# Kernel tuning notes

Measured on AMD Instinct MI355X. Metric: run time of the kernel, lower is better.

## Reference

```python
import jax, jax.numpy as jnp
import numpy as np

B, D_IN, D_OUT, M = 4096, 1024, 1024, 16
GAMMA = 2.0


def setup_inputs() -> dict:
    key = jax.random.key(0)
    ks = jax.random.split(key, 5)
    scale_in = 1.0 / np.sqrt(D_IN)
    return {
        "x": jax.random.normal(ks[0], (B, D_IN), dtype=jnp.float32),
        "W": jax.random.normal(ks[1], (M, D_IN, D_OUT), dtype=jnp.float32) * scale_in,
        "b": jax.random.normal(ks[2], (M, D_OUT), dtype=jnp.float32) * 0.01,
        "Wg": jax.random.normal(ks[3], (D_IN, M), dtype=jnp.float32) * scale_in,
        "bg": jax.random.normal(ks[4], (M,), dtype=jnp.float32) * 0.01,
    }


def reference(x, W, b, Wg, bg):
    # Gate: linear -> pow(gamma) -> normalize by row sum -> relu
    gu = x @ Wg + bg                                   # [B, M]
    gp = jnp.power(gu, GAMMA)                          # gamma = 2.0
    gates = jax.nn.relu(gp / jnp.sum(gp, axis=1, keepdims=True))  # [B, M]
    # M dense expert modules: relu(x @ W_m + b_m), gated and summed (AdditionSublayer)
    h = jax.nn.relu(jnp.einsum("bi,mio->bmo", x, W) + b)          # [B, M, D_OUT]
    return jnp.einsum("bm,bmo->bo", gates, h)                     # [B, D_OUT]
```

## Files before the change

### kernel.cpp

```cpp
#include <hip/hip_runtime.h>

typedef unsigned short u16;
typedef __attribute__((ext_vector_type(4))) float f32x4;
typedef __attribute__((ext_vector_type(8))) short bf16x8;
typedef __attribute__((ext_vector_type(4))) unsigned short u16x4;

#define NT 128

__device__ __forceinline__ u16 f2bf(float f) {
  union { float f; unsigned u; } v; v.f = f;
  unsigned r = v.u + 0x7FFFu + ((v.u >> 16) & 1u);
  return (u16)(r >> 16);
}

__device__ __forceinline__ f32x4 zero4() {
  f32x4 z; z.x = 0.f; z.y = 0.f; z.z = 0.f; z.w = 0.f; return z;
}

__global__ __launch_bounds__(256) void k_cvt_x(const float* __restrict__ x, u16* __restrict__ xb) {
  int i = blockIdx.x * 256 + threadIdx.x;
  f32x4 v = ((const f32x4*)x)[i];
  u16x4 o;
  o.x = f2bf(v.x); o.y = f2bf(v.y); o.z = f2bf(v.z); o.w = f2bf(v.w);
  ((u16x4*)xb)[i] = o;
}

__global__ __launch_bounds__(256) void k_tw(const float* __restrict__ W, u16* __restrict__ wt) {
  __shared__ float t[64][65];
  int bid = blockIdx.x;
  int e = bid >> 8, rem = bid & 255, kt = rem >> 4, nt = rem & 15;
  int tid = threadIdx.x;
  int c = tid & 63, r0 = tid >> 6;
  const float* src = W + (size_t)e * 1048576 + (size_t)(kt * 64) * 1024 + nt * 64;
  #pragma unroll
  for (int p = 0; p < 16; ++p) {
    int r = r0 + p * 4;
    t[r][c] = src[r * 1024 + c];
  }
  __syncthreads();
  u16* dst = wt + (size_t)e * 1048576 + (size_t)(nt * 64) * 1024 + kt * 64;
  #pragma unroll
  for (int p = 0; p < 16; ++p) {
    int r2 = r0 + p * 4;
    dst[r2 * 1024 + c] = f2bf(t[c][r2]);
  }
}

__global__ __launch_bounds__(256) void k_gates(const float* __restrict__ x, const float* __restrict__ Wg,
                                               const float* __restrict__ bg, float* __restrict__ gates) {
  int wid = threadIdx.x >> 6, lane = threadIdx.x & 63;
  int b = blockIdx.x * 4 + wid;
  const float* xr = x + (size_t)b * 1024;
  float acc[16];
  #pragma unroll
  for (int m = 0; m < 16; ++m) acc[m] = 0.f;
  for (int i = lane; i < 1024; i += 64) {
    float xv = xr[i];
    const f32x4* wg = (const f32x4*)(Wg + (size_t)i * 16);
    #pragma unroll
    for (int q = 0; q < 4; ++q) {
      f32x4 w = wg[q];
      acc[q*4+0] += xv * w.x; acc[q*4+1] += xv * w.y;
      acc[q*4+2] += xv * w.z; acc[q*4+3] += xv * w.w;
    }
  }
  #pragma unroll
  for (int m = 0; m < 16; ++m) {
    #pragma unroll
    for (int off = 32; off > 0; off >>= 1)
      acc[m] += __shfl_xor(acc[m], off, 64);
  }
  float tot = 0.f, gp[16];
  #pragma unroll
  for (int m = 0; m < 16; ++m) { float gu = acc[m] + bg[m]; gp[m] = gu * gu; tot += gp[m]; }
  float inv = 1.f / tot;
  if (lane == 0) {
    #pragma unroll
    for (int m = 0; m < 16; ++m) gates[(size_t)b * 16 + m] = gp[m] * inv;
  }
}

#define GLL(srcaddr, ldsaddr) \
  __builtin_amdgcn_global_load_lds((const __attribute__((address_space(1))) void*)(srcaddr), \
                                   (__attribute__((address_space(3))) void*)(ldsaddr), 16, 0, 0)

#define MFMA16(A0,A1,A2,A3,B0,B1,B2,B3) do { \
  acc[0][0] = __builtin_amdgcn_mfma_f32_16x16x32_bf16(A0, B0, acc[0][0], 0,0,0); \
  acc[0][1] = __builtin_amdgcn_mfma_f32_16x16x32_bf16(A0, B1, acc[0][1], 0,0,0); \
  acc[0][2] = __builtin_amdgcn_mfma_f32_16x16x32_bf16(A0, B2, acc[0][2], 0,0,0); \
  acc[0][3] = __builtin_amdgcn_mfma_f32_16x16x32_bf16(A0, B3, acc[0][3], 0,0,0); \
  acc[1][0] = __builtin_amdgcn_mfma_f32_16x16x32_bf16(A1, B0, acc[1][0], 0,0,0); \
  acc[1][1] = __builtin_amdgcn_mfma_f32_16x16x32_bf16(A1, B1, acc[1][1], 0,0,0); \
  acc[1][2] = __builtin_amdgcn_mfma_f32_16x16x32_bf16(A1, B2, acc[1][2], 0,0,0); \
  acc[1][3] = __builtin_amdgcn_mfma_f32_16x16x32_bf16(A1, B3, acc[1][3], 0,0,0); \
  acc[2][0] = __builtin_amdgcn_mfma_f32_16x16x32_bf16(A2, B0, acc[2][0], 0,0,0); \
  acc[2][1] = __builtin_amdgcn_mfma_f32_16x16x32_bf16(A2, B1, acc[2][1], 0,0,0); \
  acc[2][2] = __builtin_amdgcn_mfma_f32_16x16x32_bf16(A2, B2, acc[2][2], 0,0,0); \
  acc[2][3] = __builtin_amdgcn_mfma_f32_16x16x32_bf16(A2, B3, acc[2][3], 0,0,0); \
  acc[3][0] = __builtin_amdgcn_mfma_f32_16x16x32_bf16(A3, B0, acc[3][0], 0,0,0); \
  acc[3][1] = __builtin_amdgcn_mfma_f32_16x16x32_bf16(A3, B1, acc[3][1], 0,0,0); \
  acc[3][2] = __builtin_amdgcn_mfma_f32_16x16x32_bf16(A3, B2, acc[3][2], 0,0,0); \
  acc[3][3] = __builtin_amdgcn_mfma_f32_16x16x32_bf16(A3, B3, acc[3][3], 0,0,0); \
} while (0)

__global__ __launch_bounds__(512, 2)
void k_moe(const u16* __restrict__ xb, const u16* __restrict__ wt,
           const float* __restrict__ gates, const float* __restrict__ bias,
           float* __restrict__ out0, float* __restrict__ p1out) {
  __shared__ __align__(16) u16 sA[3 * 8192];
  __shared__ __align__(16) u16 sB[3 * 16384];
  __shared__ float lgat[1024];
  __shared__ float lbias[2048];

  int tid = threadIdx.x;
  int bid = blockIdx.x;
  int swz = (bid & 7) * 32 + (bid >> 3);
  int btile = swz & 31;
  int pnl = swz >> 5;
  int grp = pnl >> 2;
  int ntile = pnl & 3;
  int brow0 = btile * 128;
  int ncol0 = ntile * 256;
  int mb = grp * 8;

  int wid = tid >> 6, lane = tid & 63;
  int wm = wid >> 2, wn = wid & 3;
  int lrow = lane & 15, lk = lane >> 4;
  int sw = lrow & 7;

  const u16* asrc = xb + (size_t)brow0 * 1024;
  const u16* bsrc = wt + (size_t)mb * 1048576 + (size_t)ncol0 * 1024;

  int r0a = tid >> 3, s0a = tid & 7;
  int r1a = (512 + tid) >> 3, s1a = tid & 7;
  int sia0 = r0a * 1024 + (s0a ^ (r0a & 7)) * 8;
  int sia1 = r1a * 1024 + (s1a ^ (r1a & 7)) * 8;
  int lda0 = (wid * 64) * 8;
  int lda1 = (512 + wid * 64) * 8;
  int sib0 = sia0, sib1 = sia1;
  int r2b = (1024 + tid) >> 3;
  int r3b = (1536 + tid) >> 3;
  int sib2 = r2b * 1024 + ((tid & 7) ^ (r2b & 7)) * 8;
  int sib3 = r3b * 1024 + ((tid & 7) ^ (r3b & 7)) * 8;
  int ldb0 = lda0, ldb1 = lda1;
  int ldb2 = (1024 + wid * 64) * 8;
  int ldb3 = (1536 + wid * 64) * 8;

  int baseA = (wm * 64 + lrow) * 64;
  int baseB = (wn * 64 + lrow) * 64;
  int pa0 = baseA + ((0 + lk) ^ sw) * 8;
  int pa1 = baseA + ((4 + lk) ^ sw) * 8;
  int pb0 = baseB + ((0 + lk) ^ sw) * 8;
  int pb1 = baseB + ((4 + lk) ^ sw) * 8;

  f32x4 acc[4][4], oacc[4][4];
  #pragma unroll
  for (int i = 0; i < 4; ++i)
    #pragma unroll
    for (int j = 0; j < 4; ++j) { acc[i][j] = zero4(); oacc[i][j] = zero4(); }

  #pragma unroll
  for (int i = 0; i < 2; ++i) {
    int idx = i * 512 + tid;
    lgat[idx] = gates[(size_t)(brow0 + (idx & 127)) * 16 + mb + (idx >> 7)];
  }
  #pragma unroll
  for (int i = 0; i < 4; ++i) {
    int idx = i * 512 + tid;
    lbias[idx] = bias[(size_t)(mb + (idx >> 8)) * 1024 + ncol0 + (idx & 255)];
  }
  u16 *a0 = sA, *a1 = sA + 8192, *a2 = sA + 16384;
  u16 *b0 = sB, *b1 = sB + 16384, *b2 = sB + 32768;
  GLL(asrc + sia0, a0 + lda0); GLL(asrc + sia1, a0 + lda1);
  GLL(bsrc + sib0, b0 + ldb0); GLL(bsrc + sib1, b0 + ldb1);
  GLL(bsrc + sib2, b0 + ldb2); GLL(bsrc + sib3, b0 + ldb3);
  GLL(asrc + 64 + sia0, a1 + lda0); GLL(asrc + 64 + sia1, a1 + lda1);
  GLL(bsrc + 64 + sib0, b1 + ldb0); GLL(bsrc + 64 + sib1, b1 + ldb1);
  GLL(bsrc + 64 + sib2, b1 + ldb2); GLL(bsrc + 64 + sib3, b1 + ldb3);
  asm volatile("s_waitcnt vmcnt(6)" ::: "memory");
  __builtin_amdgcn_s_barrier();
  __builtin_amdgcn_sched_barrier(0);

  for (int t = 0; t < NT; ++t) {
    int t2 = t + 2;
    const u16* sa2 = asrc + (t2 & 15) * 64;
    const u16* sb2 = bsrc + (size_t)(t2 >> 4) * 1048576 + (t2 & 15) * 64;
    bool pf = (t2 < NT);
    bf16x8 a00, a01, a02, a03, a10, a11, a12, a13;
    bf16x8 b00, b01, b02, b03, b10, b11, b12, b13;

    a00 = *(const bf16x8*)&a0[pa0];
    a01 = *(const bf16x8*)&a0[pa0 + 1024];
    a02 = *(const bf16x8*)&a0[pa0 + 2048];
    a03 = *(const bf16x8*)&a0[pa0 + 3072];
    b00 = *(const bf16x8*)&b0[pb0];
    b01 = *(const bf16x8*)&b0[pb0 + 1024];
    b02 = *(const bf16x8*)&b0[pb0 + 2048];
    b03 = *(const bf16x8*)&b0[pb0 + 3072];
    a10 = *(const bf16x8*)&a0[pa1];
    a11 = *(const bf16x8*)&a0[pa1 + 1024];
    a12 = *(const bf16x8*)&a0[pa1 + 2048];
    a13 = *(const bf16x8*)&a0[pa1 + 3072];
    b10 = *(const bf16x8*)&b0[pb1];
    b11 = *(const bf16x8*)&b0[pb1 + 1024];
    b12 = *(const bf16x8*)&b0[pb1 + 2048];
    b13 = *(const bf16x8*)&b0[pb1 + 3072];

    if (pf) {
      GLL(sa2 + sia0, a2 + lda0); GLL(sa2 + sia1, a2 + lda1);
      GLL(sb2 + sib0, b2 + ldb0); GLL(sb2 + sib1, b2 + ldb1);
      GLL(sb2 + sib2, b2 + ldb2); GLL(sb2 + sib3, b2 + ldb3);
    }

    __builtin_amdgcn_s_setprio(1);
    MFMA16(a00, a01, a02, a03, b00, b01, b02, b03);
    MFMA16(a10, a11, a12, a13, b10, b11, b12, b13);
    __builtin_amdgcn_s_setprio(0);

    if ((t & 15) == 15) {
      int ml = t >> 4;
      float bvv[4];
      #pragma unroll
      for (int ni = 0; ni < 4; ++ni) bvv[ni] = lbias[ml * 256 + wn * 64 + ni * 16 + lrow];
      #pragma unroll
      for (int mi = 0; mi < 4; ++mi) {
        f32x4 gv = *(const f32x4*)&lgat[ml * 128 + wm * 64 + mi * 16 + lk * 4];
        #pragma unroll
        for (int ni = 0; ni < 4; ++ni) {
          #pragma unroll
          for (int j = 0; j < 4; ++j) {
            float h = acc[mi][ni][j] + bvv[ni];
            h = fmaxf(h, 0.f);
            oacc[mi][ni][j] += gv[j] * h;
          }
          acc[mi][ni] = zero4();
        }
      }
    }

    if (t < NT - 2)       asm volatile("s_waitcnt vmcnt(6)" ::: "memory");
    else if (t == NT - 2) asm volatile("s_waitcnt vmcnt(0)" ::: "memory");
    __builtin_amdgcn_s_barrier();
    __builtin_amdgcn_sched_barrier(0);

    u16* ta = a0; a0 = a1; a1 = a2; a2 = ta;
    u16* tb = b0; b0 = b1; b1 = b2; b2 = tb;
  }

  float* op = grp ? p1out : out0;
  #pragma unroll
  for (int mi = 0; mi < 4; ++mi)
    #pragma unroll
    for (int j = 0; j < 4; ++j) {
      int row = brow0 + wm * 64 + mi * 16 + lk * 4 + j;
      #pragma unroll
      for (int ni = 0; ni < 4; ++ni) {
        int col = ncol0 + wn * 64 + ni * 16 + lrow;
        op[(size_t)row * 1024 + col] = oacc[mi][ni][j];
      }
    }
}

__global__ __launch_bounds__(256) void k_add(float* __restrict__ out, const float* __restrict__ p1) {
  int i = blockIdx.x * 256 + threadIdx.x;
  f32x4 a = ((const f32x4*)out)[i];
  f32x4 b = ((const f32x4*)p1)[i];
  ((f32x4*)out)[i] = a + b;
}

extern "C" void kernel_launch(void* const* d_in, const int* in_sizes, int n_in,
                              void* d_out, int out_size, void* d_ws, size_t ws_size,
                              hipStream_t stream) {
  const float* x  = (const float*)d_in[0];
  const float* W  = (const float*)d_in[1];
  const float* b  = (const float*)d_in[2];
  const float* Wg = (const float*)d_in[3];
  const float* bg = (const float*)d_in[4];
  float* out = (float*)d_out;

  char* ws = (char*)d_ws;
  u16* xb     = (u16*)ws;
  u16* wt     = (u16*)(ws + 8388608);
  float* gts  = (float*)(ws + 41943040);
  float* p1   = (float*)(ws + 42205184);

  k_cvt_x<<<4096, 256, 0, stream>>>(x, xb);
  k_tw<<<4096, 256, 0, stream>>>(W, wt);
  k_gates<<<1024, 256, 0, stream>>>(x, Wg, bg, gts);
  k_moe<<<256, 512, 0, stream>>>(xb, wt, gts, b, out, p1);
  k_add<<<4096, 256, 0, stream>>>(out, p1);
}
```

Measured before the change: 183.7 us.

## Load x operand fragments directly from global into registers, dropping LDS staging

Removes the shared-memory buffers and global-to-LDS copies for the activation (A) operand. Each wave now loads its A fragments straight from global memory into registers, one k-step ahead of use, while the W (B) operand keeps its triple-buffered LDS pipeline. This cuts LDS traffic and footprint, but the A loads are no longer shared between waves, adding redundant global/L2 reads. The s_waitcnt now sits before the MFMAs, so the pipeline exposes global-load latency on the A path.

```diff
diff --git a/kernel.cpp b/kernel.cpp
--- a/kernel.cpp
+++ b/kernel.cpp
@@ -107,7 +107,6 @@
 void k_moe(const u16* __restrict__ xb, const u16* __restrict__ wt,
            const float* __restrict__ gates, const float* __restrict__ bias,
            float* __restrict__ out0, float* __restrict__ p1out) {
-  __shared__ __align__(16) u16 sA[3 * 8192];
   __shared__ __align__(16) u16 sB[3 * 16384];
   __shared__ float lgat[1024];
   __shared__ float lbias[2048];
@@ -128,30 +127,27 @@
   int lrow = lane & 15, lk = lane >> 4;
   int sw = lrow & 7;
 
-  const u16* asrc = xb + (size_t)brow0 * 1024;
   const u16* bsrc = wt + (size_t)mb * 1048576 + (size_t)ncol0 * 1024;
 
-  int r0a = tid >> 3, s0a = tid & 7;
-  int r1a = (512 + tid) >> 3, s1a = tid & 7;
-  int sia0 = r0a * 1024 + (s0a ^ (r0a & 7)) * 8;
-  int sia1 = r1a * 1024 + (s1a ^ (r1a & 7)) * 8;
-  int lda0 = (wid * 64) * 8;
-  int lda1 = (512 + wid * 64) * 8;
-  int sib0 = sia0, sib1 = sia1;
-  int r2b = (1024 + tid) >> 3;
-  int r3b = (1536 + tid) >> 3;
-  int sib2 = r2b * 1024 + ((tid & 7) ^ (r2b & 7)) * 8;
-  int sib3 = r3b * 1024 + ((tid & 7) ^ (r3b & 7)) * 8;
-  int ldb0 = lda0, ldb1 = lda1;
+  int g0 = tid, g1 = 512 + tid, g2 = 1024 + tid, g3 = 1536 + tid;
+  int rb0 = g0 >> 3, rb1 = g1 >> 3, rb2 = g2 >> 3, rb3 = g3 >> 3;
+  int sgb0 = rb0 * 1024 + ((g0 & 7) ^ (rb0 & 7)) * 8;
+  int sgb1 = rb1 * 1024 + ((g1 & 7) ^ (rb1 & 7)) * 8;
+  int sgb2 = rb2 * 1024 + ((g2 & 7) ^ (rb2 & 7)) * 8;
+  int sgb3 = rb3 * 1024 + ((g3 & 7) ^ (rb3 & 7)) * 8;
+  int ldb0 = (wid * 64) * 8;
+  int ldb1 = (512 + wid * 64) * 8;
   int ldb2 = (1024 + wid * 64) * 8;
   int ldb3 = (1536 + wid * 64) * 8;
 
-  int baseA = (wm * 64 + lrow) * 64;
   int baseB = (wn * 64 + lrow) * 64;
-  int pa0 = baseA + ((0 + lk) ^ sw) * 8;
-  int pa1 = baseA + ((4 + lk) ^ sw) * 8;
   int pb0 = baseB + ((0 + lk) ^ sw) * 8;
   int pb1 = baseB + ((4 + lk) ^ sw) * 8;
+
+  const u16* ar0 = xb + (size_t)(brow0 + wm * 64 +  0 + lrow) * 1024 + lk * 8;
+  const u16* ar1 = ar0 + 16 * 1024;
+  const u16* ar2 = ar0 + 32 * 1024;
+  const u16* ar3 = ar0 + 48 * 1024;
 
   f32x4 acc[4][4], oacc[4][4];
   #pragma unroll
@@ -169,53 +165,54 @@
     int idx = i * 512 + tid;
     lbias[idx] = bias[(size_t)(mb + (idx >> 8)) * 1024 + ncol0 + (idx & 255)];
   }
-  u16 *a0 = sA, *a1 = sA + 8192, *a2 = sA + 16384;
   u16 *b0 = sB, *b1 = sB + 16384, *b2 = sB + 32768;
-  GLL(asrc + sia0, a0 + lda0); GLL(asrc + sia1, a0 + lda1);
-  GLL(bsrc + sib0, b0 + ldb0); GLL(bsrc + sib1, b0 + ldb1);
-  GLL(bsrc + sib2, b0 + ldb2); GLL(bsrc + sib3, b0 + ldb3);
-  GLL(asrc + 64 + sia0, a1 + lda0); GLL(asrc + 64 + sia1, a1 + lda1);
-  GLL(bsrc + 64 + sib0, b1 + ldb0); GLL(bsrc + 64 + sib1, b1 + ldb1);
-  GLL(bsrc + 64 + sib2, b1 + ldb2); GLL(bsrc + 64 + sib3, b1 + ldb3);
-  asm volatile("s_waitcnt vmcnt(6)" ::: "memory");
+  GLL(bsrc + sgb0, b0 + ldb0); GLL(bsrc + sgb1, b0 + ldb1);
+  GLL(bsrc + sgb2, b0 + ldb2); GLL(bsrc + sgb3, b0 + ldb3);
+  GLL(bsrc + 64 + sgb0, b1 + ldb0); GLL(bsrc + 64 + sgb1, b1 + ldb1);
+  GLL(bsrc + 64 + sgb2, b1 + ldb2); GLL(bsrc + 64 + sgb3, b1 + ldb3);
+  bf16x8 fa0, fa1, fa2, fa3, ga0, ga1, ga2, ga3;
+  fa0 = *(const bf16x8*)(ar0);      ga0 = *(const bf16x8*)(ar0 + 32);
+  fa1 = *(const bf16x8*)(ar1);      ga1 = *(const bf16x8*)(ar1 + 32);
+  fa2 = *(const bf16x8*)(ar2);      ga2 = *(const bf16x8*)(ar2 + 32);
+  fa3 = *(const bf16x8*)(ar3);      ga3 = *(const bf16x8*)(ar3 + 32);
+  asm volatile("s_waitcnt vmcnt(12) lgkmcnt(0)" ::: "memory");
   __builtin_amdgcn_s_barrier();
   __builtin_amdgcn_sched_barrier(0);
 
   for (int t = 0; t < NT; ++t) {
     int t2 = t + 2;
-    const u16* sa2 = asrc + (t2 & 15) * 64;
     const u16* sb2 = bsrc + (size_t)(t2 >> 4) * 1048576 + (t2 & 15) * 64;
-    bool pf = (t2 < NT);
-    bf16x8 a00, a01, a02, a03, a10, a11, a12, a13;
     bf16x8 b00, b01, b02, b03, b10, b11, b12, b13;
 
-    a00 = *(const bf16x8*)&a0[pa0];
-    a01 = *(const bf16x8*)&a0[pa0 + 1024];
-    a02 = *(const bf16x8*)&a0[pa0 + 2048];
-    a03 = *(const bf16x8*)&a0[pa0 + 3072];
     b00 = *(const bf16x8*)&b0[pb0];
     b01 = *(const bf16x8*)&b0[pb0 + 1024];
     b02 = *(const bf16x8*)&b0[pb0 + 2048];
     b03 = *(const bf16x8*)&b0[pb0 + 3072];
-    a10 = *(const bf16x8*)&a0[pa1];
-    a11 = *(const bf16x8*)&a0[pa1 + 1024];
-    a12 = *(const bf16x8*)&a0[pa1 + 2048];
-    a13 = *(const bf16x8*)&a0[pa1 + 3072];
     b10 = *(const bf16x8*)&b0[pb1];
     b11 = *(const bf16x8*)&b0[pb1 + 1024];
     b12 = *(const bf16x8*)&b0[pb1 + 2048];
     b13 = *(const bf16x8*)&b0[pb1 + 3072];
 
-    if (pf) {
-      GLL(sa2 + sia0, a2 + lda0); GLL(sa2 + sia1, a2 + lda1);
-      GLL(sb2 + sib0, b2 + ldb0); GLL(sb2 + sib1, b2 + ldb1);
-      GLL(sb2 + sib2, b2 + ldb2); GLL(sb2 + sib3, b2 + ldb3);
-    }
+    if (t2 < NT) {
+      GLL(sb2 + sgb0, b2 + ldb0); GLL(sb2 + sgb1, b2 + ldb1);
+      GLL(sb2 + sgb2, b2 + ldb2); GLL(sb2 + sgb3, b2 + ldb3);
+    }
+
+    if (t < NT - 2) asm volatile("s_waitcnt vmcnt(4)" ::: "memory");
+    else            asm volatile("s_waitcnt vmcnt(0)" ::: "memory");
 
     __builtin_amdgcn_s_setprio(1);
-    MFMA16(a00, a01, a02, a03, b00, b01, b02, b03);
-    MFMA16(a10, a11, a12, a13, b10, b11, b12, b13);
+    MFMA16(fa0, fa1, fa2, fa3, b00, b01, b02, b03);
+    MFMA16(ga0, ga1, ga2, ga3, b10, b11, b12, b13);
     __builtin_amdgcn_s_setprio(0);
+
+    if (t + 1 < NT) {
+      int nk = ((t + 1) & 15) * 64;
+      fa0 = *(const bf16x8*)(ar0 + nk);      ga0 = *(const bf16x8*)(ar0 + nk + 32);
+      fa1 = *(const bf16x8*)(ar1 + nk);      ga1 = *(const bf16x8*)(ar1 + nk + 32);
+      fa2 = *(const bf16x8*)(ar2 + nk);      ga2 = *(const bf16x8*)(ar2 + nk + 32);
+      fa3 = *(const bf16x8*)(ar3 + nk);      ga3 = *(const bf16x8*)(ar3 + nk + 32);
+    }
 
     if ((t & 15) == 15) {
       int ml = t >> 4;
@@ -238,12 +235,9 @@
       }
     }
 
-    if (t < NT - 2)       asm volatile("s_waitcnt vmcnt(6)" ::: "memory");
-    else if (t == NT - 2) asm volatile("s_waitcnt vmcnt(0)" ::: "memory");
     __builtin_amdgcn_s_barrier();
     __builtin_amdgcn_sched_barrier(0);
 
-    u16* ta = a0; a0 = a1; a1 = a2; a2 = ta;
     u16* tb = b0; b0 = b1; b1 = b2; b2 = tb;
   }
 
```

After: 362.9 us. +97.5%, slower.

## Shrink MoE GEMM tile to 128x128 with 256 threads and double buffering

Applied to the files above, without the earlier changes.

Changes the k_moe block tile from 128x256 (8 waves, triple-buffered LDS) to 128x128 (4 waves, double-buffered LDS), and launches 512 blocks instead of 256. The smaller LDS footprint and doubled grid are meant to give better CU occupancy and load balance across the 256 CUs. In exchange, each loaded A tile is reused across fewer output columns, so global and LDS traffic per FLOP goes up. The prefetch distance also drops to one stage with a full vmcnt(0) wait every iteration, which reduces latency hiding.

```diff
diff --git a/kernel.cpp b/kernel.cpp
--- a/kernel.cpp
+++ b/kernel.cpp
@@ -103,48 +103,42 @@
   acc[3][3] = __builtin_amdgcn_mfma_f32_16x16x32_bf16(A3, B3, acc[3][3], 0,0,0); \
 } while (0)
 
-__global__ __launch_bounds__(512, 2)
+__global__ __launch_bounds__(256, 2)
 void k_moe(const u16* __restrict__ xb, const u16* __restrict__ wt,
            const float* __restrict__ gates, const float* __restrict__ bias,
            float* __restrict__ out0, float* __restrict__ p1out) {
-  __shared__ __align__(16) u16 sA[3 * 8192];
-  __shared__ __align__(16) u16 sB[3 * 16384];
+  __shared__ __align__(16) u16 sA[2 * 8192];
+  __shared__ __align__(16) u16 sB[2 * 8192];
   __shared__ float lgat[1024];
-  __shared__ float lbias[2048];
+  __shared__ float lbias[1024];
 
   int tid = threadIdx.x;
   int bid = blockIdx.x;
-  int swz = (bid & 7) * 32 + (bid >> 3);
+  int swz = (bid & 7) * 64 + (bid >> 3);
   int btile = swz & 31;
   int pnl = swz >> 5;
-  int grp = pnl >> 2;
-  int ntile = pnl & 3;
+  int ntile = pnl & 7;
+  int grp = pnl >> 3;
   int brow0 = btile * 128;
-  int ncol0 = ntile * 256;
+  int ncol0 = ntile * 128;
   int mb = grp * 8;
 
   int wid = tid >> 6, lane = tid & 63;
-  int wm = wid >> 2, wn = wid & 3;
+  int wm = wid >> 1, wn = wid & 1;
   int lrow = lane & 15, lk = lane >> 4;
   int sw = lrow & 7;
 
   const u16* asrc = xb + (size_t)brow0 * 1024;
   const u16* bsrc = wt + (size_t)mb * 1048576 + (size_t)ncol0 * 1024;
 
-  int r0a = tid >> 3, s0a = tid & 7;
-  int r1a = (512 + tid) >> 3, s1a = tid & 7;
-  int sia0 = r0a * 1024 + (s0a ^ (r0a & 7)) * 8;
-  int sia1 = r1a * 1024 + (s1a ^ (r1a & 7)) * 8;
-  int lda0 = (wid * 64) * 8;
-  int lda1 = (512 + wid * 64) * 8;
-  int sib0 = sia0, sib1 = sia1;
-  int r2b = (1024 + tid) >> 3;
-  int r3b = (1536 + tid) >> 3;
-  int sib2 = r2b * 1024 + ((tid & 7) ^ (r2b & 7)) * 8;
-  int sib3 = r3b * 1024 + ((tid & 7) ^ (r3b & 7)) * 8;
-  int ldb0 = lda0, ldb1 = lda1;
-  int ldb2 = (1024 + wid * 64) * 8;
-  int ldb3 = (1536 + wid * 64) * 8;
+  int sg[4], ldd[4];
+  #pragma unroll
+  for (int it = 0; it < 4; ++it) {
+    int idx = it * 256 + tid;
+    int r = idx >> 3, s = idx & 7;
+    sg[it] = r * 1024 + (s ^ (r & 7)) * 8;
+    ldd[it] = (it * 256 + wid * 64) * 8;
+  }
 
   int baseA = (wm * 64 + lrow) * 64;
   int baseB = (wn * 64 + lrow) * 64;
@@ -159,33 +153,30 @@
     #pragma unroll
     for (int j = 0; j < 4; ++j) { acc[i][j] = zero4(); oacc[i][j] = zero4(); }
 
-  #pragma unroll
-  for (int i = 0; i < 2; ++i) {
-    int idx = i * 512 + tid;
+  u16 *a0 = sA, *a1 = sA + 8192;
+  u16 *b0 = sB, *b1 = sB + 8192;
+
+  #pragma unroll
+  for (int it = 0; it < 4; ++it) {
+    GLL(asrc + sg[it], a0 + ldd[it]);
+    GLL(bsrc + sg[it], b0 + ldd[it]);
+  }
+  #pragma unroll
+  for (int i = 0; i < 4; ++i) {
+    int idx = i * 256 + tid;
     lgat[idx] = gates[(size_t)(brow0 + (idx & 127)) * 16 + mb + (idx >> 7)];
   }
   #pragma unroll
   for (int i = 0; i < 4; ++i) {
-    int idx = i * 512 + tid;
-    lbias[idx] = bias[(size_t)(mb + (idx >> 8)) * 1024 + ncol0 + (idx & 255)];
-  }
-  u16 *a0 = sA, *a1 = sA + 8192, *a2 = sA + 16384;
-  u16 *b0 = sB, *b1 = sB + 16384, *b2 = sB + 32768;
-  GLL(asrc + sia0, a0 + lda0); GLL(asrc + sia1, a0 + lda1);
-  GLL(bsrc + sib0, b0 + ldb0); GLL(bsrc + sib1, b0 + ldb1);
-  GLL(bsrc + sib2, b0 + ldb2); GLL(bsrc + sib3, b0 + ldb3);
-  GLL(asrc + 64 + sia0, a1 + lda0); GLL(asrc + 64 + sia1, a1 + lda1);
-  GLL(bsrc + 64 + sib0, b1 + ldb0); GLL(bsrc + 64 + sib1, b1 + ldb1);
-  GLL(bsrc + 64 + sib2, b1 + ldb2); GLL(bsrc + 64 + sib3, b1 + ldb3);
-  asm volatile("s_waitcnt vmcnt(6)" ::: "memory");
+    int idx = i * 256 + tid;
+    lbias[idx] = bias[(size_t)(mb + (idx >> 7)) * 1024 + ncol0 + (idx & 127)];
+  }
+  asm volatile("s_waitcnt vmcnt(0)" ::: "memory");
   __builtin_amdgcn_s_barrier();
   __builtin_amdgcn_sched_barrier(0);
 
   for (int t = 0; t < NT; ++t) {
-    int t2 = t + 2;
-    const u16* sa2 = asrc + (t2 & 15) * 64;
-    const u16* sb2 = bsrc + (size_t)(t2 >> 4) * 1048576 + (t2 & 15) * 64;
-    bool pf = (t2 < NT);
+    int t1 = t + 1;
     bf16x8 a00, a01, a02, a03, a10, a11, a12, a13;
     bf16x8 b00, b01, b02, b03, b10, b11, b12, b13;
 
@@ -206,10 +197,14 @@
     b12 = *(const bf16x8*)&b0[pb1 + 2048];
     b13 = *(const bf16x8*)&b0[pb1 + 3072];
 
-    if (pf) {
-      GLL(sa2 + sia0, a2 + lda0); GLL(sa2 + sia1, a2 + lda1);
-      GLL(sb2 + sib0, b2 + ldb0); GLL(sb2 + sib1, b2 + ldb1);
-      GLL(sb2 + sib2, b2 + ldb2); GLL(sb2 + sib3, b2 + ldb3);
+    if (t1 < NT) {
+      const u16* sa1 = asrc + (t1 & 15) * 64;
+      const u16* sb1 = bsrc + (size_t)(t1 >> 4) * 1048576 + (t1 & 15) * 64;
+      #pragma unroll
+      for (int it = 0; it < 4; ++it) {
+        GLL(sa1 + sg[it], a1 + ldd[it]);
+        GLL(sb1 + sg[it], b1 + ldd[it]);
+      }
     }
 
     __builtin_amdgcn_s_setprio(1);
@@ -221,7 +216,7 @@
       int ml = t >> 4;
       float bvv[4];
       #pragma unroll
-      for (int ni = 0; ni < 4; ++ni) bvv[ni] = lbias[ml * 256 + wn * 64 + ni * 16 + lrow];
+      for (int ni = 0; ni < 4; ++ni) bvv[ni] = lbias[ml * 128 + wn * 64 + ni * 16 + lrow];
       #pragma unroll
       for (int mi = 0; mi < 4; ++mi) {
         f32x4 gv = *(const f32x4*)&lgat[ml * 128 + wm * 64 + mi * 16 + lk * 4];
@@ -238,13 +233,12 @@
       }
     }
 
-    if (t < NT - 2)       asm volatile("s_waitcnt vmcnt(6)" ::: "memory");
-    else if (t == NT - 2) asm volatile("s_waitcnt vmcnt(0)" ::: "memory");
+    asm volatile("s_waitcnt vmcnt(0)" ::: "memory");
     __builtin_amdgcn_s_barrier();
     __builtin_amdgcn_sched_barrier(0);
 
-    u16* ta = a0; a0 = a1; a1 = a2; a2 = ta;
-    u16* tb = b0; b0 = b1; b1 = b2; b2 = tb;
+    u16* ta = a0; a0 = a1; a1 = ta;
+    u16* tb = b0; b0 = b1; b1 = tb;
   }
 
   float* op = grp ? p1out : out0;
@@ -287,6 +281,6 @@
   k_cvt_x<<<4096, 256, 0, stream>>>(x, xb);
   k_tw<<<4096, 256, 0, stream>>>(W, wt);
   k_gates<<<1024, 256, 0, stream>>>(x, Wg, bg, gts);
-  k_moe<<<256, 512, 0, stream>>>(xb, wt, gts, b, out, p1);
+  k_moe<<<512, 256, 0, stream>>>(xb, wt, gts, b, out, p1);
   k_add<<<4096, 256, 0, stream>>>(out, p1);
 }
```

New measurement: 185.3 us. About the same (+0.9%).
